# Kernel optimization log

Hardware: AMD Instinct MI355X
Metric: run time of the kernel (lower is better)

## Reference

```python
import jax, jax.numpy as jnp
import numpy as np

WS = 8
SHIFT = 4


def _cpb_constants(ws):
    rc = np.arange(-(ws - 1), ws, dtype=np.float32)
    gh, gw = np.meshgrid(rc, rc, indexing='ij')
    table = np.stack([gh, gw], axis=-1)[None]  # (1, 2ws-1, 2ws-1, 2)
    table = table / (ws - 1) * 8.0
    table = np.sign(table) * np.log2(np.abs(table) + 1.0) / np.log2(8.0)
    c = np.arange(ws)
    ch, cw = np.meshgrid(c, c, indexing='ij')
    flat = np.stack([ch.ravel(), cw.ravel()])  # (2, N)
    rel = (flat[:, :, None] - flat[:, None, :]).transpose(1, 2, 0).copy()
    rel[..., 0] += ws - 1
    rel[..., 1] += ws - 1
    rel[..., 0] *= 2 * ws - 1
    rpi = rel.sum(-1)  # (N, N) int
    return table.astype(np.float32), rpi


def _attn_mask(H, W, ws, s):
    # Faithful to source: middle slice is slice(-ws, +s) (empty for H>ws+s)
    img = np.zeros((H, W), np.float32)
    cnt = 0
    for hs in (slice(0, -ws), slice(-ws, s), slice(-s, None)):
        for wsl in (slice(0, -ws), slice(-ws, s), slice(-s, None)):
            img[hs, wsl] = cnt
            cnt += 1
    mw = img.reshape(H // ws, ws, W // ws, ws).transpose(0, 2, 1, 3).reshape(-1, ws * ws)
    am = mw[:, None, :] - mw[:, :, None]
    return np.where(am != 0, -100.0, 0.0).astype(np.float32)


def _dwconv(x, w):
    return jax.lax.conv_general_dilated(
        x, w, (1, 1), 'SAME',
        dimension_numbers=('NCHW', 'OIHW', 'NCHW'),
        feature_group_count=x.shape[1])


def _ln_nchw(x, g, b, eps=8e-8):
    m = x.mean(1, keepdims=True)
    v = jnp.square(x - m).mean(1, keepdims=True)
    return (x - m) / jnp.sqrt(v + eps) * g[None, :, None, None] + b[None, :, None, None]


def setup_inputs() -> dict:
    key = jax.random.key(0)
    ks = jax.random.split(key, 16)
    B, C, H, W = 16, 512, 64, 64
    nh = 16
    hid = 4 * C
    w = lambda k, s: (jax.random.normal(k, s, dtype=jnp.float32) * 0.02)
    return {
        'x': jax.random.normal(ks[0], (B, C, H, W), dtype=jnp.float32),
        'lpu_w': w(ks[1], (C, 1, 3, 3)),
        'qkv_w': w(ks[2], (3 * C, C)),
        'out_w': w(ks[3], (C, C)),
        'cpb_w1': w(ks[4], (512, 2)),
        'cpb_w2': w(ks[5], (nh, 512)),
        'logits_scale': jnp.full((nh, 1, 1), np.log(10.0), dtype=jnp.float32),
        'gamma1': jnp.ones((C,), jnp.float32),
        'beta1': jnp.zeros((C,), jnp.float32),
        'gamma2': jnp.ones((C,), jnp.float32),
        'beta2': jnp.zeros((C,), jnp.float32),
        'pw1_w': w(ks[6], (hid, C)),
        'dw_w': w(ks[7], (hid, 1, 3, 3)),
        'pw2_w': w(ks[8], (C, hid)),
        'sr_scale': jnp.ones((), jnp.float32),
        'sr_bias': jnp.zeros((), jnp.float32),
        'rs1': jnp.ones((C,), jnp.float32),
        'rs2': jnp.ones((C,), jnp.float32),
    }


def reference(x, lpu_w, qkv_w, out_w, cpb_w1, cpb_w2, logits_scale,
              gamma1, beta1, gamma2, beta2, pw1_w, dw_w, pw2_w,
              sr_scale, sr_bias, rs1, rs2):
    B, C, H, W = x.shape
    ws, s = WS, SHIFT
    nh = logits_scale.shape[0]
    hd = C // nh
    N = ws * ws
    table_np, rpi = _cpb_constants(ws)
    table = jnp.asarray(table_np)
    mask = jnp.asarray(_attn_mask(H, W, ws, s))  # (nW, N, N)

    # LPU: x + depthwise conv
    x = x + _dwconv(x, lpu_w)
    x_temp = x

    # flatten to (B, HW, C); faithful roll over dims (1,2) = tokens AND channels
    x = x.reshape(B, C, H * W).transpose(0, 2, 1)
    x = jnp.roll(x, (-s, -s), axis=(1, 2))
    # window partition
    x = x.reshape(B, H // ws, ws, W // ws, ws, C).transpose(0, 1, 3, 2, 4, 5).reshape(-1, N, C)
    Bw = x.shape[0]

    qkv = (x @ qkv_w.T).reshape(Bw, N, 3, nh, hd).transpose(2, 0, 3, 1, 4)
    q, k, v = qkv[0], qkv[1], qkv[2]
    qn = q / jnp.maximum(jnp.linalg.norm(q, axis=-1, keepdims=True), 1e-12)
    kn = k / jnp.maximum(jnp.linalg.norm(k, axis=-1, keepdims=True), 1e-12)
    scale = jnp.exp(jnp.minimum(logits_scale, jnp.log(jnp.float32(100.0))))
    attn = jnp.einsum('bhid,bhjd->bhij', qn, kn) * scale[None]

    # continuous position bias
    tbl = jax.nn.hard_swish(table @ cpb_w1.T) @ cpb_w2.T  # (1, 2ws-1, 2ws-1, nh)
    tbl = tbl.reshape(-1, nh)
    bias = tbl[rpi.reshape(-1)].reshape(N, N, nh).transpose(2, 0, 1)
    bias = 16.0 * jax.nn.sigmoid(bias)
    attn = attn + bias[None]

    nW = mask.shape[0]
    attn = (attn.reshape(Bw // nW, nW, nh, N, N) + mask[None, :, None]).reshape(-1, nh, N, N)
    # faithful: nn.Softmax(1) -> softmax over HEAD axis
    attn = jax.nn.softmax(attn, axis=1)

    o = jnp.einsum('bhij,bhjd->bhid', attn, v).transpose(0, 2, 1, 3).reshape(Bw, N, C)
    o = o @ out_w.T

    o = o.reshape(B, H // ws, ws, W // ws, ws, C)
    o = jnp.roll(o, (s, s), axis=(1, 2))  # faithful: rolls window-grid / row dims
    # faithful buggy un-partition: transpose(1,2) then reshape
    o = o.transpose(0, 2, 1, 3, 4, 5).reshape(B, C, H, W)

    x = rs1[None, :, None, None] * x_temp + _ln_nchw(o, gamma1, beta1)

    h = jnp.einsum('bchw,oc->bohw', x, pw1_w)
    h = h + _dwconv(h, dw_w)
    h = sr_scale * jnp.square(jax.nn.relu(h)) + sr_bias  # StarReLU
    y = jnp.einsum('bchw,oc->bohw', h, pw2_w)
    return rs2[None, :, None, None] * x + _ln_nchw(y, gamma2, beta2)
```

## Files before the change

### kernel.cpp

```cpp
#include <hip/hip_runtime.h>
#include <hip/hip_bf16.h>
#include <stdint.h>


typedef float f32x4 __attribute__((ext_vector_type(4)));
typedef short s16x8 __attribute__((ext_vector_type(8)));

__device__ __forceinline__ float b2f(short u) {
  return __uint_as_float(((unsigned)(unsigned short)u) << 16);
}
__device__ __forceinline__ short f2b(float f) {
  unsigned x = __float_as_uint(f);
  unsigned r = (x + 0x7fffu + ((x >> 16) & 1u)) >> 16;
  return (short)r;
}
__device__ __forceinline__ void gload16(const void* g, void* l) {
  __builtin_amdgcn_global_load_lds((const unsigned int*)g, (unsigned int*)l, 16, 0, 0);
}

__global__ __launch_bounds__(256) void k_f2b(const float* __restrict__ s,
                                             short* __restrict__ d, int n) {
  int i = blockIdx.x * 256 + threadIdx.x;
  if (i < n) d[i] = f2b(s[i]);
}

__global__ __launch_bounds__(64) void k_cpb(const float* __restrict__ w1,
                                            const float* __restrict__ w2,
                                            float* __restrict__ btab) {
  const int r = blockIdx.x;
  const int lane = threadIdx.x;
  const int ri = r / 15, rj = r % 15;
  float th = (float)(ri - 7) * (8.f / 7.f);
  float tw = (float)(rj - 7) * (8.f / 7.f);
  float gh = copysignf(log2f(fabsf(th) + 1.f) * (1.f / 3.f), th);
  float gw = copysignf(log2f(fabsf(tw) + 1.f) * (1.f / 3.f), tw);
  const int h = lane >> 2, pp = lane & 3;
  float acc = 0.f;
  for (int k = 0; k < 128; ++k) {
    int hh = pp * 128 + k;
    float a = gh * w1[hh * 2] + gw * w1[hh * 2 + 1];
    float r6 = fminf(fmaxf(a + 3.f, 0.f), 6.f);
    float hsw = a * r6 * (1.f / 6.f);
    acc += hsw * w2[h * 512 + hh];
  }
  acc += __shfl_xor(acc, 1);
  acc += __shfl_xor(acc, 2);
  if ((lane & 3) == 0) btab[h * 225 + r] = 16.f / (1.f + __expf(-acc));
}

__global__ __launch_bounds__(256) void k_lpu(const float* __restrict__ x,
                                             const float* __restrict__ lw,
                                             short* __restrict__ xt) {
  __shared__ float img[64 * 68];
  const int bc = blockIdx.x;
  const int c = bc & 511;
  const float* img_g = x + (size_t)bc * 4096;
  short* outp = xt + (size_t)bc * 4096;
  const int tid = threadIdx.x;
#pragma unroll
  for (int t = 0; t < 4; ++t) {
    int idx = t * 256 + tid;
    int h = idx >> 4, w4 = (idx & 15) * 4;
    f32x4 v = *(const f32x4*)&img_g[h * 64 + w4];
    *(f32x4*)&img[h * 68 + w4] = v;
  }
  float wreg[9];
#pragma unroll
  for (int t = 0; t < 9; ++t) wreg[t] = lw[c * 9 + t];
  __syncthreads();
  const int hb = tid >> 4, w0 = (tid & 15) * 4;
#pragma unroll
  for (int g = 0; g < 4; ++g) {
    int h = hb + g * 16;
    float row[3][6];
#pragma unroll
    for (int dr = 0; dr < 3; ++dr) {
      int hh = h - 1 + dr;
      if (hh < 0 || hh > 63) {
#pragma unroll
        for (int j = 0; j < 6; ++j) row[dr][j] = 0.f;
      } else {
        f32x4 m = *(const f32x4*)&img[hh * 68 + w0];
        row[dr][1] = m[0]; row[dr][2] = m[1]; row[dr][3] = m[2]; row[dr][4] = m[3];
        row[dr][0] = (w0 > 0) ? img[hh * 68 + w0 - 1] : 0.f;
        row[dr][5] = (w0 < 60) ? img[hh * 68 + w0 + 4] : 0.f;
      }
    }
    ushort4 o;
    unsigned short op[4];
#pragma unroll
    for (int p = 0; p < 4; ++p) {
      float acc = row[1][p + 1];
#pragma unroll
      for (int dr = 0; dr < 3; ++dr)
#pragma unroll
        for (int dc = 0; dc < 3; ++dc)
          acc += wreg[dr * 3 + dc] * row[dr][p + dc];
      op[p] = (unsigned short)f2b(acc);
    }
    o.x = op[0]; o.y = op[1]; o.z = op[2]; o.w = op[3];
    *(ushort4*)&outp[h * 64 + w0] = o;
  }
}

__global__ __launch_bounds__(256) void k_xpose(const short* __restrict__ xt,
                                               short* __restrict__ xw) {
  __shared__ short tile[64][132];
  const int tid = threadIdx.x;
  const int cq = blockIdx.x & 3;
  const int h = (blockIdx.x >> 2) & 63;
  const int b = blockIdx.x >> 8;
  const int c0 = cq * 128;
  for (int idx = tid; idx < 64 * 128; idx += 256) {
    int ww = idx & 63, cc = idx >> 6;
    int csrc = (c0 + cc + 4) & 511;
    tile[ww][cc] = xt[(((size_t)b * 512 + csrc) * 64 + h) * 64 + ww];
  }
  __syncthreads();
  for (int qd = tid; qd < 64 * 32; qd += 256) {
    int ws_ = qd >> 5, cqq = qd & 31, cc = cqq * 4;
    int t = (h * 64 + ws_ + 4092) & 4095;
    int hd = t >> 6, wd = t & 63;
    int tok = (b * 64 + (hd >> 3) * 8 + (wd >> 3)) * 64 + (hd & 7) * 8 + (wd & 7);
    ushort4 u = *(const ushort4*)&tile[ws_][cc];
    *(ushort4*)&xw[(size_t)tok * 512 + c0 + cc] = u;
  }
}

template <int EPI>
__global__ __launch_bounds__(256) void k_gemm(const short* __restrict__ A,
                                              const short* __restrict__ B,
                                              short* __restrict__ C,
                                              short* __restrict__ o4,
                                              const float* __restrict__ lsc,
                                              int N, int K, int gx) {
  __shared__ short smem[128 * 136];
  short* As = smem;
  short* Bs = smem + 128 * 64;
  const int nwg = gridDim.x;
  const int orig = blockIdx.x;
  const int wgid = (orig & 7) * (nwg >> 3) + (orig >> 3);
  const int bx = wgid % gx, by = wgid / gx;
  const int tid = threadIdx.x;
  const int lane = tid & 63, wid = tid >> 6;
  const int wm = wid >> 1, wn = wid & 1;
  const int m0 = by * 128, n0 = bx * 128;
  const f32x4 fz = {0.f, 0.f, 0.f, 0.f};
  f32x4 acc[4][4];
#pragma unroll
  for (int m = 0; m < 4; ++m)
#pragma unroll
    for (int n = 0; n < 4; ++n) acc[m][n] = fz;
  const int rst = lane >> 3;
  const int cst = (((lane & 7) ^ rst)) * 8;
  const int l15 = lane & 15, l4 = lane >> 4, l7 = lane & 7;
  for (int k0 = 0; k0 < K; k0 += 64) {
#pragma unroll
    for (int i = 0; i < 4; ++i) {
      int rb = i * 4 + wid;
      int r = rb * 8 + rst;
      gload16(A + (size_t)(m0 + r) * K + k0 + cst, As + rb * 512);
      gload16(B + (size_t)(n0 + r) * K + k0 + cst, Bs + rb * 512);
    }
    __syncthreads();
#pragma unroll
    for (int ks = 0; ks < 2; ++ks) {
      s16x8 af[4], bfr[4];
#pragma unroll
      for (int m = 0; m < 4; ++m) {
        int row = wm * 64 + m * 16 + l15;
        af[m] = *(const s16x8*)&As[row * 64 + (((ks * 4 + l4) ^ l7) * 8)];
      }
#pragma unroll
      for (int n = 0; n < 4; ++n) {
        int row = wn * 64 + n * 16 + l15;
        bfr[n] = *(const s16x8*)&Bs[row * 64 + (((ks * 4 + l4) ^ l7) * 8)];
      }
#pragma unroll
      for (int m = 0; m < 4; ++m)
#pragma unroll
        for (int n = 0; n < 4; ++n)
          acc[m][n] = __builtin_amdgcn_mfma_f32_16x16x32_bf16(af[m], bfr[n],
                                                              acc[m][n], 0, 0, 0);
    }
    __syncthreads();
  }
  if (EPI == 2 && n0 < 1024) {
    const int cb = n0 + wn * 64;
    if (cb < 1024) {
      const bool isq = cb < 512;
      float sc0 = 1.f, sc1 = 1.f;
      if (isq) {
        sc0 = __expf(fminf(lsc[cb >> 5], 4.605170185988092f));
        sc1 = __expf(fminf(lsc[(cb >> 5) + 1], 4.605170185988092f));
      }
#pragma unroll
      for (int m = 0; m < 4; ++m)
#pragma unroll
        for (int np = 0; np < 2; ++np)
#pragma unroll
          for (int r = 0; r < 4; ++r) {
            float s0 = acc[m][2 * np][r], s1 = acc[m][2 * np + 1][r];
            float ss = s0 * s0 + s1 * s1;
            ss += __shfl_xor(ss, 1);
            ss += __shfl_xor(ss, 2);
            ss += __shfl_xor(ss, 4);
            ss += __shfl_xor(ss, 8);
            float mul = (np ? sc1 : sc0) / fmaxf(sqrtf(ss), 1e-12f);
            acc[m][2 * np][r] = s0 * mul;
            acc[m][2 * np + 1][r] = s1 * mul;
          }
    }
  }
  short* ct = smem;
#pragma unroll
  for (int m = 0; m < 4; ++m)
#pragma unroll
    for (int n = 0; n < 4; ++n)
#pragma unroll
      for (int r = 0; r < 4; ++r) {
        int lr = wm * 64 + m * 16 + l4 * 4 + r;
        int lc = wn * 64 + n * 16 + l15;
        ct[lr * 136 + lc] = f2b(acc[m][n][r]);
      }
  __syncthreads();
  const int colslot = tid & 15;
#pragma unroll
  for (int ps = 0; ps < 8; ++ps) {
    int lr = (tid >> 4) + ps * 16;
    s16x8 v = *(const s16x8*)&ct[lr * 136 + colslot * 8];
    int grow = m0 + lr;
    int gcol = n0 + colslot * 8;
    if (EPI != 1) {
      *(s16x8*)&C[(size_t)grow * N + gcol] = v;
    } else {
      int win = grow >> 6, nn = grow & 63;
      int b = win >> 6, whs = (win >> 3) & 7, wws = win & 7;
      int ih = nn >> 3, iw = nn & 7;
      int wh = (whs + 4) & 7, ww = (wws + 4) & 7;
      int cp = ww * 64 + wh * 8 + ih;
      int hp = iw * 8 + (gcol >> 6);
      int wp = gcol & 63;
      *(s16x8*)&o4[(((size_t)b * 512 + cp) * 64 + hp) * 64 + wp] = v;
    }
  }
}

__global__ __launch_bounds__(256) void k_attn(const short* __restrict__ qkv,
                                              const float* __restrict__ btab_g,
                                              short* __restrict__ o_ws) {
  __shared__ float btab[3600];
  __shared__ short vts[2][2048];
  __shared__ short pts[4][1024];
  const int tid = threadIdx.x, lane = tid & 63, wid = tid >> 6;
  const int win = blockIdx.x;
  const int l15 = lane & 15, l4 = lane >> 4;
  const int qrow0 = wid * 16;
  for (int i = tid; i < 3600; i += 256) btab[i] = btab_g[i];
  int baddr[4][4];
#pragma unroll
  for (int n = 0; n < 4; ++n)
#pragma unroll
    for (int r = 0; r < 4; ++r) {
      int i_ = qrow0 + l4 * 4 + r, j_ = n * 16 + l15;
      int dih = (i_ >> 3) - (j_ >> 3) + 7;
      int diw = (i_ & 7) - (j_ & 7) + 7;
      baddr[n][r] = dih * 15 + diw;
    }
  __syncthreads();
  const short* base = qkv + (size_t)win * 64 * 1536;
  const f32x4 fz = {0.f, 0.f, 0.f, 0.f};
  f32x4 sump[4] = {fz, fz, fz, fz};
#pragma unroll 2
  for (int h = 0; h < 16; ++h) {
    s16x8 qf = *(const s16x8*)(base + (size_t)(qrow0 + l15) * 1536 + h * 32 + l4 * 8);
#pragma unroll
    for (int n = 0; n < 4; ++n) {
      s16x8 kf = *(const s16x8*)(base + (size_t)(n * 16 + l15) * 1536 + 512 + h * 32 + l4 * 8);
      f32x4 s = __builtin_amdgcn_mfma_f32_16x16x32_bf16(qf, kf, fz, 0, 0, 0);
#pragma unroll
      for (int r = 0; r < 4; ++r)
        sump[n][r] += __expf(s[r] + btab[h * 225 + baddr[n][r]]);
    }
  }
  f32x4 rden[4];
#pragma unroll
  for (int n = 0; n < 4; ++n)
#pragma unroll
    for (int r = 0; r < 4; ++r) rden[n][r] = 1.f / sump[n][r];
  char* pt = (char*)pts[wid];
  {
    int j = tid & 63, d0 = (tid >> 6) * 8;
    s16x8 vv = *(const s16x8*)(base + (size_t)j * 1536 + 1024 + d0);
#pragma unroll
    for (int jj = 0; jj < 8; ++jj) {
      int d = d0 + jj;
      *(short*)((char*)vts[0] + ((d * 128 + j * 2) ^ ((d & 7) << 4))) = vv[jj];
    }
  }
  __syncthreads();
  for (int h = 0; h < 16; ++h) {
    const char* vcur = (const char*)vts[h & 1];
    if (h < 15) {
      int j = tid & 63, d0 = (tid >> 6) * 8;
      s16x8 vv = *(const s16x8*)(base + (size_t)j * 1536 + 1024 + (h + 1) * 32 + d0);
      char* vnxt = (char*)vts[(h + 1) & 1];
#pragma unroll
      for (int jj = 0; jj < 8; ++jj) {
        int d = d0 + jj;
        *(short*)(vnxt + ((d * 128 + j * 2) ^ ((d & 7) << 4))) = vv[jj];
      }
    }
    s16x8 qf = *(const s16x8*)(base + (size_t)(qrow0 + l15) * 1536 + h * 32 + l4 * 8);
#pragma unroll
    for (int n = 0; n < 4; ++n) {
      s16x8 kf = *(const s16x8*)(base + (size_t)(n * 16 + l15) * 1536 + 512 + h * 32 + l4 * 8);
      f32x4 s = __builtin_amdgcn_mfma_f32_16x16x32_bf16(qf, kf, fz, 0, 0, 0);
#pragma unroll
      for (int r = 0; r < 4; ++r) {
        float pv = __expf(s[r] + btab[h * 225 + baddr[n][r]]) * rden[n][r];
        int i_loc = l4 * 4 + r, j_ = n * 16 + l15;
        *(short*)(pt + ((i_loc * 128 + j_ * 2) ^ ((i_loc & 7) << 4))) = f2b(pv);
      }
    }
    f32x4 oacc[2] = {fz, fz};
#pragma unroll
    for (int kb = 0; kb < 2; ++kb) {
      s16x8 af = *(const s16x8*)(pt + ((l15 * 128 + kb * 64 + l4 * 16) ^ ((l15 & 7) << 4)));
#pragma unroll
      for (int db = 0; db < 2; ++db) {
        int d = db * 16 + l15;
        s16x8 bf = *(const s16x8*)(vcur + ((d * 128 + kb * 64 + l4 * 16) ^ ((d & 7) << 4)));
        oacc[db] = __builtin_amdgcn_mfma_f32_16x16x32_bf16(af, bf, oacc[db], 0, 0, 0);
      }
    }
    short* ob = o_ws + ((size_t)win * 64 + qrow0) * 512 + h * 32;
#pragma unroll
    for (int db = 0; db < 2; ++db)
#pragma unroll
      for (int r = 0; r < 4; ++r)
        ob[(size_t)(l4 * 4 + r) * 512 + db * 16 + l15] = f2b(oacc[db][r]);
    __syncthreads();
  }
}

__global__ __launch_bounds__(256) void k_ln1(const short* __restrict__ o4,
                                             const short* __restrict__ xt,
                                             const float* __restrict__ g1,
                                             const float* __restrict__ b1,
                                             const float* __restrict__ rs1,
                                             short* __restrict__ x2h) {
  __shared__ float reds[4][64], redq[4][64];
  __shared__ float mean_s[64], rstd_s[64];
  __shared__ short tile[128][66];
  const int tid = threadIdx.x;
  const int b = blockIdx.x >> 6, hp = blockIdx.x & 63;
  const int w = tid & 63, part = tid >> 6;
  const short* base = o4 + (size_t)b * 512 * 4096 + hp * 64;
  float s = 0.f, q = 0.f;
  for (int c = part; c < 512; c += 4) {
    float v = b2f(base[(size_t)c * 4096 + w]);
    s += v; q += v * v;
  }
  reds[part][w] = s; redq[part][w] = q;
  __syncthreads();
  if (tid < 64) {
    float S = 0.f, Q = 0.f;
    for (int i = 0; i < 4; ++i) { S += reds[i][tid]; Q += redq[i][tid]; }
    float m = S * (1.f / 512.f);
    float var = Q * (1.f / 512.f) - m * m;
    mean_s[tid] = m;
    rstd_s[tid] = rsqrtf(var + 8e-8f);
  }
  __syncthreads();
  const short* xtb = xt + (size_t)b * 512 * 4096 + hp * 64;
  for (int c0 = 0; c0 < 512; c0 += 128) {
    for (int cc = part; cc < 128; cc += 4) {
      int c = c0 + cc;
      float v = b2f(base[(size_t)c * 4096 + w]);
      float ln = (v - mean_s[w]) * rstd_s[w] * g1[c] + b1[c];
      float xv = rs1[c] * b2f(xtb[(size_t)c * 4096 + w]) + ln;
      tile[cc][w] = f2b(xv);
    }
    __syncthreads();
    short* xh = x2h + ((size_t)blockIdx.x * 64) * 512 + c0;
    for (int qd = tid; qd < 64 * 32; qd += 256) {
      int w_ = qd >> 5, cq = qd & 31, cc = cq * 4;
      ushort4 u;
      u.x = (unsigned short)tile[cc][w_];
      u.y = (unsigned short)tile[cc + 1][w_];
      u.z = (unsigned short)tile[cc + 2][w_];
      u.w = (unsigned short)tile[cc + 3][w_];
      *(ushort4*)&xh[(size_t)w_ * 512 + cc] = u;
    }
    __syncthreads();
  }
}

__global__ __launch_bounds__(256) void k_dwc2(const short* __restrict__ h1,
                                              const float* __restrict__ dw,
                                              const float* __restrict__ srs_p,
                                              const float* __restrict__ srb_p,
                                              short* __restrict__ h2) {
  __shared__ short tile[6 * 64 * 64];
  const int tid = threadIdx.x;
  const int cblk = blockIdx.x & 31;
  const int hq = (blockIdx.x >> 5) & 15;
  const int b = blockIdx.x >> 9;
  const int c0 = cblk * 64;
  const int h0 = hq * 4;
  for (int t = 0; t < 12; ++t) {
    int idx = t * 256 + tid;
    int cg = idx & 7;
    int wl = (idx >> 3) & 63;
    int rl = idx >> 9;
    int hr = h0 - 1 + rl;
    s16x8 v = {0, 0, 0, 0, 0, 0, 0, 0};
    if (hr >= 0 && hr < 64)
      v = *(const s16x8*)&h1[((size_t)b * 4096 + hr * 64 + wl) * 2048 + c0 + cg * 8];
    *(s16x8*)&tile[(rl * 64 + wl) * 64 + (cg ^ (wl & 7)) * 8] = v;
  }
  const int cg = tid & 7;
  const int wq = tid >> 3;
  float wt[9][8];
#pragma unroll
  for (int j = 0; j < 8; ++j) {
    int cch = c0 + cg * 8 + j;
#pragma unroll
    for (int t = 0; t < 9; ++t) wt[t][j] = dw[cch * 9 + t];
  }
  const float srs = *srs_p, srb = *srb_p;
  __syncthreads();
#pragma unroll
  for (int it = 0; it < 8; ++it) {
    int wl = wq + (it & 1) * 32;
    int rl = it >> 1;
    s16x8 ctr = *(const s16x8*)&tile[((rl + 1) * 64 + wl) * 64 + (cg ^ (wl & 7)) * 8];
    float acc[8];
#pragma unroll
    for (int j = 0; j < 8; ++j) acc[j] = b2f(ctr[j]);
#pragma unroll
    for (int dh = -1; dh <= 1; ++dh) {
      int row = rl + 1 + dh;
#pragma unroll
      for (int dwi = -1; dwi <= 1; ++dwi) {
        int wn = wl + dwi;
        if (wn < 0 || wn > 63) continue;
        s16x8 v = *(const s16x8*)&tile[(row * 64 + wn) * 64 + (cg ^ (wn & 7)) * 8];
        const float* wrow = wt[(dh + 1) * 3 + dwi + 1];
#pragma unroll
        for (int j = 0; j < 8; ++j) acc[j] += wrow[j] * b2f(v[j]);
      }
    }
    s16x8 o;
#pragma unroll
    for (int j = 0; j < 8; ++j) {
      float rr = fmaxf(acc[j], 0.f);
      o[j] = f2b(srs * rr * rr + srb);
    }
    *(s16x8*)&h2[((size_t)b * 4096 + (h0 + rl) * 64 + wl) * 2048 + c0 + cg * 8] = o;
  }
}

__global__ __launch_bounds__(256) void k_final(const short* __restrict__ y,
                                               const short* __restrict__ x2h,
                                               const float* __restrict__ g2,
                                               const float* __restrict__ b2p,
                                               const float* __restrict__ rs2,
                                               float* __restrict__ out) {
  __shared__ short yt[64][132];
  __shared__ short xt2[64][132];
  __shared__ float reds[4][64], redq[4][64];
  __shared__ float mean_s[64], rstd_s[64];
  const int tid = threadIdx.x;
  const int b = blockIdx.x >> 6, hh = blockIdx.x & 63;
  const int w = tid & 63, part = tid >> 6;
  const short* yb = y + (size_t)blockIdx.x * 64 * 512;
  const short* xb = x2h + (size_t)blockIdx.x * 64 * 512;
  float s = 0.f, q = 0.f;
  for (int c0 = 0; c0 < 512; c0 += 128) {
    for (int qd = tid; qd < 64 * 32; qd += 256) {
      int w_ = qd >> 5, g = qd & 31;
      *(ushort4*)&yt[w_][g * 4] = *(const ushort4*)&yb[(size_t)w_ * 512 + c0 + g * 4];
    }
    __syncthreads();
    for (int cc = part * 32; cc < part * 32 + 32; ++cc) {
      float v = b2f(yt[w][cc]);
      s += v; q += v * v;
    }
    __syncthreads();
  }
  reds[part][w] = s; redq[part][w] = q;
  __syncthreads();
  if (tid < 64) {
    float S = 0.f, Q = 0.f;
    for (int i = 0; i < 4; ++i) { S += reds[i][tid]; Q += redq[i][tid]; }
    float m = S * (1.f / 512.f);
    float var = Q * (1.f / 512.f) - m * m;
    mean_s[tid] = m;
    rstd_s[tid] = rsqrtf(var + 8e-8f);
  }
  __syncthreads();
  float* ob = out + (size_t)b * 512 * 4096 + hh * 64;
  for (int c0 = 0; c0 < 512; c0 += 128) {
    for (int qd = tid; qd < 64 * 32; qd += 256) {
      int w_ = qd >> 5, g = qd & 31;
      *(ushort4*)&yt[w_][g * 4] = *(const ushort4*)&yb[(size_t)w_ * 512 + c0 + g * 4];
      *(ushort4*)&xt2[w_][g * 4] = *(const ushort4*)&xb[(size_t)w_ * 512 + c0 + g * 4];
    }
    __syncthreads();
    for (int it = 0; it < 32; ++it) {
      int c = c0 + it * 4 + part;
      float yv = b2f(yt[w][c - c0]);
      float lnv = (yv - mean_s[w]) * rstd_s[w] * g2[c] + b2p[c];
      float xv = b2f(xt2[w][c - c0]);
      ob[(size_t)c * 4096 + w] = rs2[c] * xv + lnv;
    }
    __syncthreads();
  }
}

extern "C" void kernel_launch(void* const* d_in, const int* in_sizes, int n_in,
                              void* d_out, int out_size, void* d_ws, size_t ws_size,
                              hipStream_t stream) {
  (void)in_sizes; (void)n_in; (void)out_size; (void)ws_size;
  const float* x      = (const float*)d_in[0];
  const float* lpu_w  = (const float*)d_in[1];
  const float* qkv_w  = (const float*)d_in[2];
  const float* out_w  = (const float*)d_in[3];
  const float* cpb_w1 = (const float*)d_in[4];
  const float* cpb_w2 = (const float*)d_in[5];
  const float* lsc    = (const float*)d_in[6];
  const float* g1     = (const float*)d_in[7];
  const float* b1     = (const float*)d_in[8];
  const float* g2     = (const float*)d_in[9];
  const float* b2v    = (const float*)d_in[10];
  const float* pw1_w  = (const float*)d_in[11];
  const float* dw_w   = (const float*)d_in[12];
  const float* pw2_w  = (const float*)d_in[13];
  const float* srs    = (const float*)d_in[14];
  const float* srb    = (const float*)d_in[15];
  const float* rs1    = (const float*)d_in[16];
  const float* rs2    = (const float*)d_in[17];

  char* ws = (char*)d_ws;
  float* btab   = (float*)(ws + 0);
  short* wbq    = (short*)(ws + 16384);
  short* wbo    = (short*)(ws + 1589248);
  short* wb1    = (short*)(ws + 2113536);
  short* wb2    = (short*)(ws + 4210688);
  short* x_temp = (short*)(ws + 8388608);
  short* xw     = (short*)(ws + 75497472);
  short* qkv    = (short*)(ws + 142606336);
  short* o_ws   = (short*)(ws + 343932928);
  short* o4     = (short*)(ws + 75497472);
  short* x2h    = (short*)(ws + 142606336);
  short* h1     = (short*)(ws + 209715200);
  short* h2     = (short*)(ws + 8388608);
  short* yb     = (short*)(ws + 343932928);

  k_f2b<<<3072, 256, 0, stream>>>(qkv_w, wbq, 786432);
  k_f2b<<<1024, 256, 0, stream>>>(out_w, wbo, 262144);
  k_f2b<<<4096, 256, 0, stream>>>(pw1_w, wb1, 1048576);
  k_f2b<<<4096, 256, 0, stream>>>(pw2_w, wb2, 1048576);
  k_cpb<<<225, 64, 0, stream>>>(cpb_w1, cpb_w2, btab);
  k_lpu<<<8192, 256, 0, stream>>>(x, lpu_w, x_temp);
  k_xpose<<<4096, 256, 0, stream>>>(x_temp, xw);
  k_gemm<2><<<6144, 256, 0, stream>>>(xw, wbq, qkv, nullptr, lsc, 1536, 512, 12);
  k_attn<<<1024, 256, 0, stream>>>(qkv, btab, o_ws);
  k_gemm<1><<<2048, 256, 0, stream>>>(o_ws, wbo, nullptr, o4, nullptr, 512, 512, 4);
  k_ln1<<<1024, 256, 0, stream>>>(o4, x_temp, g1, b1, rs1, x2h);
  for (int ch = 0; ch < 2; ++ch) {
    const size_t tok0 = (size_t)ch * 8 * 4096;
    k_gemm<0><<<4096, 256, 0, stream>>>(x2h + tok0 * 512, wb1, h1, nullptr, nullptr, 2048, 512, 16);
    k_dwc2<<<4096, 256, 0, stream>>>(h1, dw_w, srs, srb, h2);
    k_gemm<0><<<1024, 256, 0, stream>>>(h2, wb2, yb + tok0 * 512, nullptr, nullptr, 512, 2048, 4);
  }
  k_final<<<1024, 256, 0, stream>>>(yb, x2h, g2, b2v, rs2, (float*)d_out);
}
```

Baseline: 1.223 ms.

## Shrink GEMM LDS, split epilogue in halves, fuse weight conversions, precompute load pointers

Shrinks the GEMM shared-memory buffer from 128x136 to 2x128x64 shorts by staging the epilogue output tile in two 64-row halves, which allows more workgroups per CU. It also precomputes global load pointers outside the K loop and merges the four weight fp32-to-bf16 conversion launches into one vectorised kernel. The f2b rounding now uses the library intrinsic. The split epilogue adds a barrier and a second pass in exchange for the lower LDS footprint.

```diff
diff --git a/kernel.cpp b/kernel.cpp
--- a/kernel.cpp
+++ b/kernel.cpp
@@ -10,18 +10,35 @@
   return __uint_as_float(((unsigned)(unsigned short)u) << 16);
 }
 __device__ __forceinline__ short f2b(float f) {
-  unsigned x = __float_as_uint(f);
-  unsigned r = (x + 0x7fffu + ((x >> 16) & 1u)) >> 16;
-  return (short)r;
+  __hip_bfloat16 h = __float2bfloat16(f);
+  short s;
+  __builtin_memcpy(&s, &h, 2);
+  return s;
 }
 __device__ __forceinline__ void gload16(const void* g, void* l) {
   __builtin_amdgcn_global_load_lds((const unsigned int*)g, (unsigned int*)l, 16, 0, 0);
 }
 
-__global__ __launch_bounds__(256) void k_f2b(const float* __restrict__ s,
-                                             short* __restrict__ d, int n) {
-  int i = blockIdx.x * 256 + threadIdx.x;
-  if (i < n) d[i] = f2b(s[i]);
+__global__ __launch_bounds__(256) void k_f2b4(const float* __restrict__ s0, short* __restrict__ d0,
+                                              const float* __restrict__ s1, short* __restrict__ d1,
+                                              const float* __restrict__ s2, short* __restrict__ d2,
+                                              const float* __restrict__ s3, short* __restrict__ d3) {
+  int b = blockIdx.x;
+  const float* s;
+  short* d;
+  int base;
+  if (b < 768) { s = s0; d = d0; base = b * 1024; }
+  else if (b < 1024) { s = s1; d = d1; base = (b - 768) * 1024; }
+  else if (b < 2048) { s = s2; d = d2; base = (b - 1024) * 1024; }
+  else { s = s3; d = d3; base = (b - 2048) * 1024; }
+  int i = base + threadIdx.x * 4;
+  f32x4 v = *(const f32x4*)&s[i];
+  ushort4 o;
+  o.x = (unsigned short)f2b(v[0]);
+  o.y = (unsigned short)f2b(v[1]);
+  o.z = (unsigned short)f2b(v[2]);
+  o.w = (unsigned short)f2b(v[3]);
+  *(ushort4*)&d[i] = o;
 }
 
 __global__ __launch_bounds__(64) void k_cpb(const float* __restrict__ w1,
@@ -134,7 +151,7 @@
                                               short* __restrict__ o4,
                                               const float* __restrict__ lsc,
                                               int N, int K, int gx) {
-  __shared__ short smem[128 * 136];
+  __shared__ short smem[2 * 128 * 64];
   short* As = smem;
   short* Bs = smem + 128 * 64;
   const int nwg = gridDim.x;
@@ -152,15 +169,24 @@
 #pragma unroll
     for (int n = 0; n < 4; ++n) acc[m][n] = fz;
   const int rst = lane >> 3;
-  const int cst = (((lane & 7) ^ rst)) * 8;
+  const int cst = ((lane & 7) ^ rst) * 8;
   const int l15 = lane & 15, l4 = lane >> 4, l7 = lane & 7;
+  const short* ap[4];
+  const short* bp[4];
+#pragma unroll
+  for (int i = 0; i < 4; ++i) {
+    int r = (i * 4 + wid) * 8 + rst;
+    ap[i] = A + (size_t)(m0 + r) * K + cst;
+    bp[i] = B + (size_t)(n0 + r) * K + cst;
+  }
   for (int k0 = 0; k0 < K; k0 += 64) {
 #pragma unroll
     for (int i = 0; i < 4; ++i) {
       int rb = i * 4 + wid;
-      int r = rb * 8 + rst;
-      gload16(A + (size_t)(m0 + r) * K + k0 + cst, As + rb * 512);
-      gload16(B + (size_t)(n0 + r) * K + k0 + cst, Bs + rb * 512);
+      gload16(ap[i], As + rb * 512);
+      gload16(bp[i], Bs + rb * 512);
+      ap[i] += 64;
+      bp[i] += 64;
     }
     __syncthreads();
 #pragma unroll
@@ -213,35 +239,41 @@
     }
   }
   short* ct = smem;
-#pragma unroll
-  for (int m = 0; m < 4; ++m)
-#pragma unroll
-    for (int n = 0; n < 4; ++n)
-#pragma unroll
-      for (int r = 0; r < 4; ++r) {
-        int lr = wm * 64 + m * 16 + l4 * 4 + r;
-        int lc = wn * 64 + n * 16 + l15;
-        ct[lr * 136 + lc] = f2b(acc[m][n][r]);
-      }
-  __syncthreads();
   const int colslot = tid & 15;
 #pragma unroll
-  for (int ps = 0; ps < 8; ++ps) {
-    int lr = (tid >> 4) + ps * 16;
-    s16x8 v = *(const s16x8*)&ct[lr * 136 + colslot * 8];
-    int grow = m0 + lr;
-    int gcol = n0 + colslot * 8;
-    if (EPI != 1) {
-      *(s16x8*)&C[(size_t)grow * N + gcol] = v;
-    } else {
-      int win = grow >> 6, nn = grow & 63;
-      int b = win >> 6, whs = (win >> 3) & 7, wws = win & 7;
-      int ih = nn >> 3, iw = nn & 7;
-      int wh = (whs + 4) & 7, ww = (wws + 4) & 7;
-      int cp = ww * 64 + wh * 8 + ih;
-      int hp = iw * 8 + (gcol >> 6);
-      int wp = gcol & 63;
-      *(s16x8*)&o4[(((size_t)b * 512 + cp) * 64 + hp) * 64 + wp] = v;
+  for (int p = 0; p < 2; ++p) {
+    if (p) __syncthreads();
+#pragma unroll
+    for (int mm = 0; mm < 2; ++mm) {
+      int m = p * 2 + mm;
+#pragma unroll
+      for (int n = 0; n < 4; ++n)
+#pragma unroll
+        for (int r = 0; r < 4; ++r) {
+          int lrow = wm * 32 + mm * 16 + l4 * 4 + r;
+          int lc = wn * 64 + n * 16 + l15;
+          ct[lrow * 136 + lc] = f2b(acc[m][n][r]);
+        }
+    }
+    __syncthreads();
+#pragma unroll
+    for (int ps = 0; ps < 4; ++ps) {
+      int lr = (tid >> 4) + ps * 16;
+      s16x8 v = *(const s16x8*)&ct[lr * 136 + colslot * 8];
+      int grow = m0 + (lr >> 5) * 64 + p * 32 + (lr & 31);
+      int gcol = n0 + colslot * 8;
+      if (EPI != 1) {
+        *(s16x8*)&C[(size_t)grow * N + gcol] = v;
+      } else {
+        int win = grow >> 6, nn = grow & 63;
+        int b = win >> 6, whs = (win >> 3) & 7, wws = win & 7;
+        int ih = nn >> 3, iw = nn & 7;
+        int wh = (whs + 4) & 7, ww = (wws + 4) & 7;
+        int cp = ww * 64 + wh * 8 + ih;
+        int hp = iw * 8 + (gcol >> 6);
+        int wp = gcol & 63;
+        *(s16x8*)&o4[(((size_t)b * 512 + cp) * 64 + hp) * 64 + wp] = v;
+      }
     }
   }
 }
@@ -559,10 +591,7 @@
   short* h2     = (short*)(ws + 8388608);
   short* yb     = (short*)(ws + 343932928);
 
-  k_f2b<<<3072, 256, 0, stream>>>(qkv_w, wbq, 786432);
-  k_f2b<<<1024, 256, 0, stream>>>(out_w, wbo, 262144);
-  k_f2b<<<4096, 256, 0, stream>>>(pw1_w, wb1, 1048576);
-  k_f2b<<<4096, 256, 0, stream>>>(pw2_w, wb2, 1048576);
+  k_f2b4<<<3072, 256, 0, stream>>>(qkv_w, wbq, out_w, wbo, pw1_w, wb1, pw2_w, wb2);
   k_cpb<<<225, 64, 0, stream>>>(cpb_w1, cpb_w2, btab);
   k_lpu<<<8192, 256, 0, stream>>>(x, lpu_w, x_temp);
   k_xpose<<<4096, 256, 0, stream>>>(x_temp, xw);
```

New measurement: 1.169 ms. -4.4%, faster.
